# Kernel tuning notes

Measured on AMD Instinct MI355X. Metric: run time of the kernel, lower is better.

## Reference

```python
import jax, jax.numpy as jnp
import numpy as np
from jax import lax

N, F_IN, HID, OUT, L, K = 50000, 128, 128, 64, 3, 9
E = 600000
PAD = (K - 1) // 2
BN_EPS = 1e-5


def setup_inputs() -> dict:
    key = jax.random.key(0)
    ks = jax.random.split(key, 16)
    return {
        "x": jax.random.normal(ks[0], (N, F_IN), jnp.float32),
        "edge_index": jax.random.randint(ks[1], (2, E), 0, N, jnp.int64),
        "tw": jax.random.normal(ks[2], (L, HID, F_IN, K), jnp.float32) * 0.05,
        "tb": jax.random.normal(ks[3], (L, HID), jnp.float32) * 0.05,
        "wl": jax.random.normal(ks[4], (L, HID, HID), jnp.float32) * 0.05,
        "bl": jax.random.normal(ks[5], (L, HID), jnp.float32) * 0.05,
        "wr": jax.random.normal(ks[6], (L, HID, HID), jnp.float32) * 0.05,
        "bn_g": jax.random.uniform(ks[7], (L, HID), jnp.float32, 0.5, 1.5),
        "bn_b": jax.random.normal(ks[8], (L, HID), jnp.float32) * 0.05,
        "bn_m": jax.random.normal(ks[9], (L, HID), jnp.float32) * 0.05,
        "bn_v": jax.random.uniform(ks[10], (L, HID), jnp.float32, 0.5, 1.5),
        "clf_w": jax.random.normal(ks[11], (OUT, HID), jnp.float32) * 0.05,
        "clf_b": jax.random.normal(ks[12], (OUT,), jnp.float32) * 0.05,
    }


def reference(x, edge_index, tw, tb, wl, bl, wr, bn_g, bn_b, bn_m, bn_v, clf_w, clf_b):
    # Eval mode: dropout = identity, BatchNorm uses running stats.
    src, dst = edge_index[0], edge_index[1]
    n = x.shape[0]
    # mean-aggregation denominator (PyG SAGEConv 'mean'); isolated nodes -> 0
    deg = jax.ops.segment_sum(jnp.ones((src.shape[0],), x.dtype), dst, num_segments=n)
    inv_deg = jnp.where(deg > 0, 1.0 / jnp.maximum(deg, 1.0), 0.0)[:, None]  # [N,1]
    for i in range(L):
        # temporal Conv1d over the NODE axis: [N,C] -> [1,C,N]
        h = lax.conv_general_dilated(
            x.T[None], tw[i], window_strides=(1,), padding=[(PAD, PAD)],
            dimension_numbers=("NCH", "OIH", "NCH"))
        h = jax.nn.relu(h + tb[i][None, :, None])[0].T  # [N, HID]
        # SAGEConv: lin_l(mean_j h_j) + lin_r(h_i)
        agg = jax.ops.segment_sum(h[src], dst, num_segments=n) * inv_deg
        h = agg @ wl[i].T + bl[i] + h @ wr[i].T
        # BatchNorm1d (eval) + ReLU
        h = bn_g[i] * (h - bn_m[i]) * lax.rsqrt(bn_v[i] + BN_EPS) + bn_b[i]
        x = jax.nn.relu(h)
    logits = x @ clf_w.T + clf_b
    return jax.nn.log_softmax(logits, axis=1)
```

## Files before the change

kernel.cpp:

```cpp
#include <hip/hip_runtime.h>
#include <cstddef>
#include <cstdint>


#define N_NODES 50000
#define FDIM    128
#define OUTC    64
#define NLAYER  3
#define KW      9
#define PADW    4
#define NEDGE   600000
#define BN_EPS  1e-5f

typedef short bf16x8 __attribute__((ext_vector_type(8)));
typedef float f32x4  __attribute__((ext_vector_type(4)));

__device__ __forceinline__ float relu_(float v){ return v > 0.f ? v : 0.f; }

__device__ __forceinline__ unsigned short bf_rne(float x){
  unsigned u = __float_as_uint(x);
  unsigned r = u + 0x7fff + ((u >> 16) & 1);
  return (unsigned short)(r >> 16);
}
__device__ __forceinline__ unsigned short bf_hi(float x, float& rem){
  unsigned short h = bf_rne(x);
  rem = x - __uint_as_float(((unsigned)h) << 16);
  return h;
}
__device__ __forceinline__ float bf2f(unsigned short u){
  return __uint_as_float(((unsigned)u) << 16);
}
__device__ __forceinline__ void cvt8(const float4& f0, const float4& f1, int4& hv, int4& lv){
  float f[8] = {f0.x,f0.y,f0.z,f0.w,f1.x,f1.y,f1.z,f1.w};
  unsigned short h[8], l[8];
  #pragma unroll
  for (int i=0;i<8;i++){ float r; h[i] = bf_hi(f[i], r); l[i] = bf_rne(r); }
  hv.x = (int)((unsigned)h[0] | ((unsigned)h[1]<<16));
  hv.y = (int)((unsigned)h[2] | ((unsigned)h[3]<<16));
  hv.z = (int)((unsigned)h[4] | ((unsigned)h[5]<<16));
  hv.w = (int)((unsigned)h[6] | ((unsigned)h[7]<<16));
  lv.x = (int)((unsigned)l[0] | ((unsigned)l[1]<<16));
  lv.y = (int)((unsigned)l[2] | ((unsigned)l[3]<<16));
  lv.z = (int)((unsigned)l[4] | ((unsigned)l[5]<<16));
  lv.w = (int)((unsigned)l[6] | ((unsigned)l[7]<<16));
}


__global__ void k_detect(const int* __restrict__ ei, int* __restrict__ flag){
  int t = threadIdx.x;
  unsigned long long b = __ballot(ei[2*t+1] == 0);
  if (t == 0) flag[0] = (b == ~0ull) ? 1 : 0;
}

__global__ void k_zero(int* __restrict__ p, int n){
  int i = blockIdx.x*256 + threadIdx.x;
  if (i < n) p[i] = 0;
}

__global__ void k_deg(const int* __restrict__ ei, const int* __restrict__ flag, int* __restrict__ deg){
  int e = blockIdx.x*256 + threadIdx.x;
  if (e >= NEDGE) return;
  int d = flag[0] ? ei[2*(NEDGE+e)] : ei[NEDGE+e];
  atomicAdd(&deg[d], 1);
}

__global__ void k_scan1(const int* __restrict__ deg, int* __restrict__ rp, int* __restrict__ bsums){
  __shared__ int sd[256];
  int t = threadIdx.x, base = blockIdx.x*1024 + t*4;
  int v0=0,v1=0,v2=0,v3=0;
  if (base+3 < N_NODES){ int4 q = *(const int4*)(deg+base); v0=q.x; v1=q.y; v2=q.z; v3=q.w; }
  else {
    if (base   < N_NODES) v0 = deg[base];
    if (base+1 < N_NODES) v1 = deg[base+1];
    if (base+2 < N_NODES) v2 = deg[base+2];
    if (base+3 < N_NODES) v3 = deg[base+3];
  }
  int s = v0+v1+v2+v3;
  sd[t] = s; __syncthreads();
  #pragma unroll
  for (int o=1;o<256;o<<=1){
    int x = (t>=o) ? sd[t-o] : 0;
    __syncthreads();
    sd[t] += x;
    __syncthreads();
  }
  int excl = sd[t]-s;
  if (base   < N_NODES) rp[base  ] = excl;
  if (base+1 < N_NODES) rp[base+1] = excl+v0;
  if (base+2 < N_NODES) rp[base+2] = excl+v0+v1;
  if (base+3 < N_NODES) rp[base+3] = excl+v0+v1+v2;
  if (t==255) bsums[blockIdx.x] = sd[255];
}

__global__ void k_scan2(int* __restrict__ bsums, int nb){
  if (threadIdx.x==0 && blockIdx.x==0){
    int run = 0;
    for (int i=0;i<nb;i++){ int x = bsums[i]; bsums[i] = run; run += x; }
  }
}

__global__ void k_scan3(int* __restrict__ rp, int* __restrict__ cur, float* __restrict__ idg,
                        const int* __restrict__ deg, const int* __restrict__ bsums){
  int i = blockIdx.x*256 + threadIdx.x;
  if (i < N_NODES){
    int r = rp[i] + bsums[i>>10];
    rp[i] = r; cur[i] = r;
    int d = deg[i];
    idg[i] = (d>0) ? 1.0f/(float)d : 0.0f;
  } else if (i == N_NODES){
    rp[N_NODES] = NEDGE;
  }
}

__global__ void k_fill(const int* __restrict__ ei, const int* __restrict__ flag,
                       int* __restrict__ cur, int* __restrict__ col){
  int e = blockIdx.x*256 + threadIdx.x;
  if (e >= NEDGE) return;
  int s,d;
  if (flag[0]){ s = ei[2*e]; d = ei[2*(NEDGE+e)]; }
  else        { s = ei[e];   d = ei[NEDGE+e];   }
  int pos = atomicAdd(&cur[d], 1);
  col[pos] = s;
}


__global__ void k_pack(const float* __restrict__ tw, const float* __restrict__ wl,
                       const float* __restrict__ wr, const float* __restrict__ cw,
                       unsigned short* __restrict__ wp, unsigned short* __restrict__ wg,
                       float* __restrict__ cwt){
  int i = blockIdx.x*256 + threadIdx.x;
  const int T1v = 442368, T2v = 98304, T3v = 8192;
  if (i < T1v){
    int e = i & 7, lane = (i>>3)&63, ob = (i>>9)&7, cb = (i>>12)&3, kl = i>>14;
    int k = kl % KW, l = kl / KW;
    int o = ob*16 + (lane&15), c = cb*32 + (lane>>4)*8 + e;
    float v = tw[(((l*128+o)*128+c)*KW) + k];
    float rem; unsigned short hi = bf_hi(v, rem); unsigned short lo = bf_rne(rem);
    int chunk = (((l*KW+k)*4+cb)*8+ob)*2;
    wp[(size_t)chunk*512 + lane*8 + e]     = hi;
    wp[(size_t)(chunk+1)*512 + lane*8 + e] = lo;
  } else if (i < T1v+T2v){
    int i2 = i - T1v;
    int e = i2 & 7, lane = (i2>>3)&63, ob = (i2>>9)&7, ks = (i2>>12)&7, l = i2>>15;
    int o = ob*16 + (lane&15), j = ks*32 + (lane>>4)*8 + e;
    float v = (j < 128) ? wl[(l*128+o)*128 + j] : wr[(l*128+o)*128 + (j-128)];
    float rem; unsigned short hi = bf_hi(v, rem); unsigned short lo = bf_rne(rem);
    int chunk = ((l*8+ks)*8+ob)*2;
    wg[(size_t)chunk*512 + lane*8 + e]     = hi;
    wg[(size_t)(chunk+1)*512 + lane*8 + e] = lo;
  } else if (i < T1v+T2v+T3v){
    int j3 = i - (T1v+T2v);
    int o = j3 & 63, c = j3 >> 6;
    cwt[j3] = cw[o*128 + c];
  }
}


#define CROWS 72

__global__ __launch_bounds__(256, 4) void k_convm(const float* __restrict__ xf,
                                                  const unsigned short* __restrict__ xhi,
                                                  const unsigned short* __restrict__ xlo,
                                                  const int use_planes,
                                                  const unsigned short* __restrict__ wpl,
                                                  const float* __restrict__ tb,
                                                  unsigned short* __restrict__ hhi,
                                                  unsigned short* __restrict__ hlo){
  __shared__ unsigned short sh[2*CROWS*64];
  const int t = threadIdx.x;
  const int n0 = blockIdx.x*64;
  const int l = t & 63, w = t >> 6;
  const int l15 = l & 15, kg = l >> 4;
  const bf16x8* Bp = (const bf16x8*)wpl;

  f32x4 acc[4][2];
  #pragma unroll
  for (int rf=0;rf<4;rf++){ acc[rf][0] = (f32x4)0.f; acc[rf][1] = (f32x4)0.f; }

  bf16x8 B00, B01, B10, B11;
  {
    int ch = ((0*4+0)*8 + 2*w)*2;
    B00 = Bp[ch*64 + l]; B01 = Bp[(ch+1)*64 + l];
    B10 = Bp[(ch+2)*64 + l]; B11 = Bp[(ch+3)*64 + l];
  }

  for (int half = 0; half < 2; ++half){
    if (half) __syncthreads();
    for (int u = t; u < CROWS*8; u += 256){
      int row = u >> 3, c8 = u & 7;
      int gn = n0 - PADW + row;
      int4 hv = make_int4(0,0,0,0), lv = make_int4(0,0,0,0);
      if (gn >= 0 && gn < N_NODES){
        if (use_planes){
          size_t o = (size_t)gn*FDIM + half*64 + c8*8;
          hv = *(const int4*)(xhi + o);
          lv = *(const int4*)(xlo + o);
        } else {
          const float* src = xf + (size_t)gn*FDIM + half*64 + c8*8;
          float4 f0 = *(const float4*)src, f1 = *(const float4*)(src+4);
          cvt8(f0, f1, hv, lv);
        }
      }
      int idx = row*64 + ((c8 ^ (row&7)) << 3);
      *(int4*)&sh[idx] = hv;
      *(int4*)&sh[CROWS*64 + idx] = lv;
    }
    __syncthreads();

    for (int kk = 0; kk < 18; ++kk){
      int k = kk >> 1, cb2 = kk & 1;
      bf16x8 Bc00=B00, Bc01=B01, Bc10=B10, Bc11=B11;
      {
        int it = half*18 + kk;
        int itn = (it+1 < 36) ? it+1 : it;
        int halfn = itn/18, kkn = itn%18;
        int kn = kkn>>1, cb2n = kkn&1, cbgn = halfn*2 + cb2n;
        int ch = ((kn*4+cbgn)*8 + 2*w)*2;
        B00 = Bp[ch*64 + l]; B01 = Bp[(ch+1)*64 + l];
        B10 = Bp[(ch+2)*64 + l]; B11 = Bp[(ch+3)*64 + l];
      }
      int cc3 = cb2*4 + kg;
      int swz = ((cc3 ^ ((l15 + k) & 7)) << 3);
      int base = (l15 + k)*64 + swz;
      #pragma unroll
      for (int rf = 0; rf < 4; ++rf){
        int idx = base + rf*16*64;
        bf16x8 Ah = *(const bf16x8*)&sh[idx];
        bf16x8 Al = *(const bf16x8*)&sh[CROWS*64 + idx];
        acc[rf][0] = __builtin_amdgcn_mfma_f32_16x16x32_bf16(Ah, Bc00, acc[rf][0], 0,0,0);
        acc[rf][0] = __builtin_amdgcn_mfma_f32_16x16x32_bf16(Ah, Bc01, acc[rf][0], 0,0,0);
        acc[rf][0] = __builtin_amdgcn_mfma_f32_16x16x32_bf16(Al, Bc00, acc[rf][0], 0,0,0);
        acc[rf][1] = __builtin_amdgcn_mfma_f32_16x16x32_bf16(Ah, Bc10, acc[rf][1], 0,0,0);
        acc[rf][1] = __builtin_amdgcn_mfma_f32_16x16x32_bf16(Ah, Bc11, acc[rf][1], 0,0,0);
        acc[rf][1] = __builtin_amdgcn_mfma_f32_16x16x32_bf16(Al, Bc10, acc[rf][1], 0,0,0);
      }
    }
  }

  int o0 = w*32 + l15, o1 = o0 + 16;
  float tb0 = tb[o0], tb1 = tb[o1];
  #pragma unroll
  for (int rf = 0; rf < 4; ++rf){
    #pragma unroll
    for (int j = 0; j < 4; ++j){
      int n = n0 + rf*16 + kg*4 + j;
      if (n < N_NODES){
        float v0 = relu_(acc[rf][0][j] + tb0);
        float v1 = relu_(acc[rf][1][j] + tb1);
        float r0, r1;
        unsigned short h0 = bf_hi(v0, r0), h1 = bf_hi(v1, r1);
        size_t b = (size_t)n*FDIM;
        hhi[b+o0] = h0; hlo[b+o0] = bf_rne(r0);
        hhi[b+o1] = h1; hlo[b+o1] = bf_rne(r1);
      }
    }
  }
}


__global__ __launch_bounds__(256) void k_agg(const unsigned short* __restrict__ hhi,
                                             const int* __restrict__ rp,
                                             const int* __restrict__ col,
                                             const float* __restrict__ idg,
                                             unsigned short* __restrict__ ahi,
                                             unsigned short* __restrict__ alo){
  int n = blockIdx.x*4 + (threadIdx.x>>6);
  int lane = threadIdx.x & 63;
  int half = lane >> 5, li = lane & 31;
  if (n >= N_NODES) return;
  int s0 = rp[n], s1 = rp[n+1];
  float a0=0.f, a1=0.f, a2=0.f, a3=0.f;
  int e = s0 + half;
  for (; e + 2 < s1; e += 4){
    int sA = col[e], sB = col[e+2];
    ushort4 vA = *(const ushort4*)(hhi + (size_t)sA*FDIM + li*4);
    ushort4 vB = *(const ushort4*)(hhi + (size_t)sB*FDIM + li*4);
    a0 += bf2f(vA.x) + bf2f(vB.x);
    a1 += bf2f(vA.y) + bf2f(vB.y);
    a2 += bf2f(vA.z) + bf2f(vB.z);
    a3 += bf2f(vA.w) + bf2f(vB.w);
  }
  for (; e < s1; e += 2){
    int s = col[e];
    ushort4 v = *(const ushort4*)(hhi + (size_t)s*FDIM + li*4);
    a0 += bf2f(v.x); a1 += bf2f(v.y); a2 += bf2f(v.z); a3 += bf2f(v.w);
  }
  a0 += __shfl_xor(a0, 32);
  a1 += __shfl_xor(a1, 32);
  a2 += __shfl_xor(a2, 32);
  a3 += __shfl_xor(a3, 32);
  float wv = idg[n];
  a0 *= wv; a1 *= wv; a2 *= wv; a3 *= wv;
  float r0,r1,r2,r3;
  unsigned short h0 = bf_hi(a0,r0), h1 = bf_hi(a1,r1), h2 = bf_hi(a2,r2), h3 = bf_hi(a3,r3);
  size_t b = (size_t)n*FDIM + li*4;
  if (half == 0){
    ushort4 o; o.x=h0; o.y=h1; o.z=h2; o.w=h3;
    *(ushort4*)(ahi + b) = o;
  } else {
    ushort4 o; o.x=bf_rne(r0); o.y=bf_rne(r1); o.z=bf_rne(r2); o.w=bf_rne(r3);
    *(ushort4*)(alo + b) = o;
  }
}


__global__ __launch_bounds__(256, 4) void k_gemmm(const unsigned short* __restrict__ ahi,
                                                  const unsigned short* __restrict__ alo,
                                                  const unsigned short* __restrict__ hhi,
                                                  const unsigned short* __restrict__ hlo,
                                                  const unsigned short* __restrict__ wgl,
                                                  const float* __restrict__ bl,
                                                  const float* __restrict__ bng, const float* __restrict__ bnb,
                                                  const float* __restrict__ bnm, const float* __restrict__ bnv,
                                                  unsigned short* __restrict__ xhi,
                                                  unsigned short* __restrict__ xlo){
  __shared__ unsigned short sh[2*64*64];
  const int t = threadIdx.x;
  const int n0 = blockIdx.x*64;
  const int l = t & 63, w = t >> 6;
  const int l15 = l & 15, kg = l >> 4;
  const bf16x8* Bp = (const bf16x8*)wgl;

  f32x4 acc[4][2];
  #pragma unroll
  for (int rf=0;rf<4;rf++){ acc[rf][0] = (f32x4)0.f; acc[rf][1] = (f32x4)0.f; }

  bf16x8 B00, B01, B10, B11;
  {
    int ch = (0*8 + 2*w)*2;
    B00 = Bp[ch*64 + l]; B01 = Bp[(ch+1)*64 + l];
    B10 = Bp[(ch+2)*64 + l]; B11 = Bp[(ch+3)*64 + l];
  }

  for (int p = 0; p < 4; ++p){
    if (p) __syncthreads();
    const unsigned short* shi = (p >= 2) ? hhi : ahi;
    const unsigned short* slo = (p >= 2) ? hlo : alo;
    int ch0 = (p & 1)*64;
    for (int u = t; u < 64*8; u += 256){
      int row = u >> 3, c8 = u & 7;
      int gn = n0 + row;
      int4 hv = make_int4(0,0,0,0), lv = make_int4(0,0,0,0);
      if (gn < N_NODES){
        size_t o = (size_t)gn*FDIM + ch0 + c8*8;
        hv = *(const int4*)(shi + o);
        lv = *(const int4*)(slo + o);
      }
      int idx = row*64 + ((c8 ^ (row&7)) << 3);
      *(int4*)&sh[idx] = hv;
      *(int4*)&sh[64*64 + idx] = lv;
    }
    __syncthreads();

    for (int cb2 = 0; cb2 < 2; ++cb2){
      bf16x8 Bc00=B00, Bc01=B01, Bc10=B10, Bc11=B11;
      {
        int ks = p*2 + cb2;
        int ksn = (ks+1 < 8) ? ks+1 : ks;
        int ch = (ksn*8 + 2*w)*2;
        B00 = Bp[ch*64 + l]; B01 = Bp[(ch+1)*64 + l];
        B10 = Bp[(ch+2)*64 + l]; B11 = Bp[(ch+3)*64 + l];
      }
      int cc3 = cb2*4 + kg;
      int swz = ((cc3 ^ (l15 & 7)) << 3);
      int base = l15*64 + swz;
      #pragma unroll
      for (int rf = 0; rf < 4; ++rf){
        int idx = base + rf*16*64;
        bf16x8 Ah = *(const bf16x8*)&sh[idx];
        bf16x8 Al = *(const bf16x8*)&sh[64*64 + idx];
        acc[rf][0] = __builtin_amdgcn_mfma_f32_16x16x32_bf16(Ah, Bc00, acc[rf][0], 0,0,0);
        acc[rf][0] = __builtin_amdgcn_mfma_f32_16x16x32_bf16(Ah, Bc01, acc[rf][0], 0,0,0);
        acc[rf][0] = __builtin_amdgcn_mfma_f32_16x16x32_bf16(Al, Bc00, acc[rf][0], 0,0,0);
        acc[rf][1] = __builtin_amdgcn_mfma_f32_16x16x32_bf16(Ah, Bc10, acc[rf][1], 0,0,0);
        acc[rf][1] = __builtin_amdgcn_mfma_f32_16x16x32_bf16(Ah, Bc11, acc[rf][1], 0,0,0);
        acc[rf][1] = __builtin_amdgcn_mfma_f32_16x16x32_bf16(Al, Bc10, acc[rf][1], 0,0,0);
      }
    }
  }

  int o0 = w*32 + l15, o1 = o0 + 16;
  float s0 = bng[o0]*rsqrtf(bnv[o0]+BN_EPS);
  float c0 = bnb[o0] + s0*(bl[o0]-bnm[o0]);
  float s1 = bng[o1]*rsqrtf(bnv[o1]+BN_EPS);
  float c1 = bnb[o1] + s1*(bl[o1]-bnm[o1]);
  #pragma unroll
  for (int rf = 0; rf < 4; ++rf){
    #pragma unroll
    for (int j = 0; j < 4; ++j){
      int n = n0 + rf*16 + kg*4 + j;
      if (n < N_NODES){
        float v0 = relu_(s0*acc[rf][0][j] + c0);
        float v1 = relu_(s1*acc[rf][1][j] + c1);
        float r0, r1;
        unsigned short h0 = bf_hi(v0, r0), h1 = bf_hi(v1, r1);
        size_t b = (size_t)n*FDIM;
        xhi[b+o0] = h0; xlo[b+o0] = bf_rne(r0);
        xhi[b+o1] = h1; xlo[b+o1] = bf_rne(r1);
      }
    }
  }
}


__global__ __launch_bounds__(256) void k_clf(const unsigned short* __restrict__ xhi,
                                             const unsigned short* __restrict__ xlo,
                                             const float* __restrict__ cwt,
                                             const float* __restrict__ cb, float* __restrict__ out){
  __shared__ float As[128][68];
  __shared__ float mxl[64];
  const int t = threadIdx.x, n0 = blockIdx.x*64;
  const int ng = t & 15, og = t>>4;
  float acc[4][4];
  #pragma unroll
  for (int i=0;i<4;i++)
    #pragma unroll
    for (int j=0;j<4;j++) acc[i][j] = 0.f;

  for (int u=t; u<64*16; u+=256){
    int row = u>>4, c16 = u&15;
    int gn = n0 + row;
    int4 hv = make_int4(0,0,0,0), lv = make_int4(0,0,0,0);
    if (gn < N_NODES){
      size_t o = (size_t)gn*FDIM + c16*8;
      hv = *(const int4*)(xhi + o);
      lv = *(const int4*)(xlo + o);
    }
    const unsigned short* hs = (const unsigned short*)&hv;
    const unsigned short* ls = (const unsigned short*)&lv;
    #pragma unroll
    for (int j=0;j<8;j++) As[c16*8+j][row] = bf2f(hs[j]) + bf2f(ls[j]);
  }
  __syncthreads();
  #pragma unroll 2
  for (int c=0;c<128;c++){
    float aa[4] = {As[c][ng], As[c][ng+16], As[c][ng+32], As[c][ng+48]};
    float4 b = *(const float4*)(cwt + c*64 + og*4);
    float bb[4] = {b.x,b.y,b.z,b.w};
    #pragma unroll
    for (int i=0;i<4;i++)
      #pragma unroll
      for (int j=0;j<4;j++) acc[i][j] = fmaf(aa[i], bb[j], acc[i][j]);
  }
  __syncthreads();
  float4 cb4 = *(const float4*)(cb + og*4);
  float cbv[4] = {cb4.x,cb4.y,cb4.z,cb4.w};
  #pragma unroll
  for (int i=0;i<4;i++)
    #pragma unroll
    for (int j=0;j<4;j++) As[ng+16*i][og*4+j] = acc[i][j] + cbv[j];
  __syncthreads();
  if (t < 64){
    float mx = -1e30f;
    #pragma unroll 8
    for (int o=0;o<64;o++) mx = fmaxf(mx, As[t][o]);
    float se = 0.f;
    #pragma unroll 8
    for (int o=0;o<64;o++) se += expf(As[t][o]-mx);
    mxl[t] = mx + logf(se);
  }
  __syncthreads();
  #pragma unroll
  for (int v=0;v<4;v++){
    int q = t + v*256;
    int r = q>>4, o4 = (q&15)*4;
    int n = n0 + r;
    if (n < N_NODES){
      float4 L = *(const float4*)&As[r][o4];
      float m = mxl[r];
      float4 wv; wv.x = L.x-m; wv.y = L.y-m; wv.z = L.z-m; wv.w = L.w-m;
      *(float4*)(out + (size_t)n*OUTC + o4) = wv;
    }
  }
}


extern "C" void kernel_launch(void* const* d_in, const int* in_sizes, int n_in,
                              void* d_out, int out_size, void* d_ws, size_t ws_size,
                              hipStream_t stream) {
  const float* x   = (const float*)d_in[0];
  const int*   ei  = (const int*)  d_in[1];
  const float* tw  = (const float*)d_in[2];
  const float* tb  = (const float*)d_in[3];
  const float* wl  = (const float*)d_in[4];
  const float* bl  = (const float*)d_in[5];
  const float* wr  = (const float*)d_in[6];
  const float* bng = (const float*)d_in[7];
  const float* bnb = (const float*)d_in[8];
  const float* bnm = (const float*)d_in[9];
  const float* bnv = (const float*)d_in[10];
  const float* cw  = (const float*)d_in[11];
  const float* cb  = (const float*)d_in[12];
  float* out = (float*)d_out;
  char* ws = (char*)d_ws;

  auto align256 = [](size_t v){ return (v + 255) & ~(size_t)255; };
  size_t off = 0;
  auto take = [&](size_t bytes){ size_t o = off; off += align256(bytes); return o; };
  const size_t PLANE = (size_t)N_NODES*FDIM*2;
  unsigned short* xhi = (unsigned short*)(ws + take(PLANE));
  unsigned short* xlo = (unsigned short*)(ws + take(PLANE));
  unsigned short* hhi = (unsigned short*)(ws + take(PLANE));
  unsigned short* hlo = (unsigned short*)(ws + take(PLANE));
  unsigned short* ahi = (unsigned short*)(ws + take(PLANE));
  unsigned short* alo = (unsigned short*)(ws + take(PLANE));
  unsigned short* wp  = (unsigned short*)(ws + take((size_t)884736*2));
  unsigned short* wg  = (unsigned short*)(ws + take((size_t)196608*2));
  float* cwt   = (float*)(ws + take((size_t)128*64*4));
  int*   deg   = (int*)  (ws + take((size_t)N_NODES*4));
  int*   rp    = (int*)  (ws + take((size_t)(N_NODES+1)*4));
  int*   cur   = (int*)  (ws + take((size_t)N_NODES*4));
  int*   col   = (int*)  (ws + take((size_t)NEDGE*4));
  float* idg   = (float*)(ws + take((size_t)N_NODES*4));
  int*   bsums = (int*)  (ws + take(256));
  int*   flag  = (int*)  (ws + take(256));
  (void)ws_size; (void)in_sizes; (void)n_in; (void)out_size;

  const int NB_N   = (N_NODES + 255)/256;
  const int NB_E   = (NEDGE   + 255)/256;
  const int NB_SC  = (N_NODES + 1023)/1024;
  const int NB_T64 = (N_NODES + 63)/64;
  const int NB_PK  = (442368 + 98304 + 8192)/256;

  k_detect<<<1, 64, 0, stream>>>(ei, flag);
  k_zero  <<<NB_N, 256, 0, stream>>>(deg, N_NODES);
  k_deg   <<<NB_E, 256, 0, stream>>>(ei, flag, deg);
  k_scan1 <<<NB_SC, 256, 0, stream>>>(deg, rp, bsums);
  k_scan2 <<<1, 64, 0, stream>>>(bsums, NB_SC);
  k_scan3 <<<NB_N+1, 256, 0, stream>>>(rp, cur, idg, deg, bsums);
  k_fill  <<<NB_E, 256, 0, stream>>>(ei, flag, cur, col);
  k_pack  <<<NB_PK, 256, 0, stream>>>(tw, wl, wr, cw, wp, wg, cwt);

  for (int l=0; l<NLAYER; l++){
    k_convm<<<NB_T64, 256, 0, stream>>>(x, xhi, xlo, (l>0) ? 1 : 0,
                                        wp + (size_t)l*294912, tb + l*128, hhi, hlo);
    k_agg  <<<N_NODES/4, 256, 0, stream>>>(hhi, rp, col, idg, ahi, alo);
    k_gemmm<<<NB_T64, 256, 0, stream>>>(ahi, alo, hhi, hlo, wg + (size_t)l*65536,
                                        bl + l*128, bng + l*128, bnb + l*128,
                                        bnm + l*128, bnv + l*128, xhi, xlo);
  }
  k_clf<<<NB_T64, 256, 0, stream>>>(xhi, xlo, cwt, cb, out);
}
```

Measured before the change: 474.8 us.

## Prefetch next shared-memory stage into registers and double-buffer weight fragments

In the temporal-conv and SAGE linear kernels, the global loads for the next input stage are now issued into registers before the MFMA loop on the current stage, then written to shared memory after a barrier. This lets global-memory latency overlap with matrix compute instead of stalling at each stage boundary. Weight fragments are also double-buffered two iterations ahead, using two register sets. The cost is higher register pressure, which may reduce occupancy, plus an extra barrier per stage.

Result: slower. 502.1 us (+5.7%).

```diff
diff --git a/kernel.cpp b/kernel.cpp
--- a/kernel.cpp
+++ b/kernel.cpp
@@ -177,63 +177,113 @@
   #pragma unroll
   for (int rf=0;rf<4;rf++){ acc[rf][0] = (f32x4)0.f; acc[rf][1] = (f32x4)0.f; }
 
-  bf16x8 B00, B01, B10, B11;
-  {
-    int ch = ((0*4+0)*8 + 2*w)*2;
-    B00 = Bp[ch*64 + l]; B01 = Bp[(ch+1)*64 + l];
-    B10 = Bp[(ch+2)*64 + l]; B11 = Bp[(ch+3)*64 + l];
-  }
-
-  for (int half = 0; half < 2; ++half){
-    if (half) __syncthreads();
-    for (int u = t; u < CROWS*8; u += 256){
-      int row = u >> 3, c8 = u & 7;
-      int gn = n0 - PADW + row;
-      int4 hv = make_int4(0,0,0,0), lv = make_int4(0,0,0,0);
-      if (gn >= 0 && gn < N_NODES){
-        if (use_planes){
-          size_t o = (size_t)gn*FDIM + half*64 + c8*8;
-          hv = *(const int4*)(xhi + o);
-          lv = *(const int4*)(xlo + o);
-        } else {
-          const float* src = xf + (size_t)gn*FDIM + half*64 + c8*8;
-          float4 f0 = *(const float4*)src, f1 = *(const float4*)(src+4);
+  int4 sA[3], sB[3];
+  auto stage_load = [&](int half){
+    #pragma unroll
+    for (int i=0;i<3;i++){
+      int u = t + i*256;
+      sA[i] = make_int4(0,0,0,0); sB[i] = make_int4(0,0,0,0);
+      if (u < CROWS*8){
+        int row = u>>3, c8 = u&7;
+        int gn = n0 - PADW + row;
+        if (gn >= 0 && gn < N_NODES){
+          if (use_planes){
+            size_t o = (size_t)gn*FDIM + half*64 + c8*8;
+            sA[i] = *(const int4*)(xhi + o);
+            sB[i] = *(const int4*)(xlo + o);
+          } else {
+            const float* src = xf + (size_t)gn*FDIM + half*64 + c8*8;
+            sA[i] = *(const int4*)src;
+            sB[i] = *(const int4*)(src+4);
+          }
+        }
+      }
+    }
+  };
+  auto stage_write = [&](){
+    #pragma unroll
+    for (int i=0;i<3;i++){
+      int u = t + i*256;
+      if (u < CROWS*8){
+        int row = u>>3, c8 = u&7;
+        int idx = row*64 + ((c8 ^ (row&7)) << 3);
+        int4 hv, lv;
+        if (use_planes){ hv = sA[i]; lv = sB[i]; }
+        else {
+          float4 f0 = *(float4*)&sA[i], f1 = *(float4*)&sB[i];
           cvt8(f0, f1, hv, lv);
         }
-      }
-      int idx = row*64 + ((c8 ^ (row&7)) << 3);
-      *(int4*)&sh[idx] = hv;
-      *(int4*)&sh[CROWS*64 + idx] = lv;
-    }
-    __syncthreads();
-
-    for (int kk = 0; kk < 18; ++kk){
-      int k = kk >> 1, cb2 = kk & 1;
-      bf16x8 Bc00=B00, Bc01=B01, Bc10=B10, Bc11=B11;
+        *(int4*)&sh[idx] = hv;
+        *(int4*)&sh[CROWS*64 + idx] = lv;
+      }
+    }
+  };
+
+  auto chbase = [&](int it)->int{
+    int halfn = it/18, kkn = it%18;
+    int kn = kkn>>1, cb2n = kkn&1, cbgn = halfn*2 + cb2n;
+    return ((kn*4+cbgn)*8 + 2*w)*2;
+  };
+
+  bf16x8 BA0,BA1,BA2,BA3, BB0,BB1,BB2,BB3;
+  { int ch = chbase(0);
+    BA0 = Bp[ch*64+l]; BA1 = Bp[(ch+1)*64+l]; BA2 = Bp[(ch+2)*64+l]; BA3 = Bp[(ch+3)*64+l]; }
+  { int ch = chbase(1);
+    BB0 = Bp[ch*64+l]; BB1 = Bp[(ch+1)*64+l]; BB2 = Bp[(ch+2)*64+l]; BB3 = Bp[(ch+3)*64+l]; }
+
+  stage_load(0);
+  stage_write();
+  __syncthreads();
+
+  for (int half = 0; half < 2; ++half){
+    if (half == 0) stage_load(1);
+    for (int kk2 = 0; kk2 < 18; kk2 += 2){
+      int k = kk2 >> 1;
+      int rowk = l15 + k;
       {
-        int it = half*18 + kk;
-        int itn = (it+1 < 36) ? it+1 : it;
-        int halfn = itn/18, kkn = itn%18;
-        int kn = kkn>>1, cb2n = kkn&1, cbgn = halfn*2 + cb2n;
-        int ch = ((kn*4+cbgn)*8 + 2*w)*2;
-        B00 = Bp[ch*64 + l]; B01 = Bp[(ch+1)*64 + l];
-        B10 = Bp[(ch+2)*64 + l]; B11 = Bp[(ch+3)*64 + l];
-      }
-      int cc3 = cb2*4 + kg;
-      int swz = ((cc3 ^ ((l15 + k) & 7)) << 3);
-      int base = (l15 + k)*64 + swz;
-      #pragma unroll
-      for (int rf = 0; rf < 4; ++rf){
-        int idx = base + rf*16*64;
-        bf16x8 Ah = *(const bf16x8*)&sh[idx];
-        bf16x8 Al = *(const bf16x8*)&sh[CROWS*64 + idx];
-        acc[rf][0] = __builtin_amdgcn_mfma_f32_16x16x32_bf16(Ah, Bc00, acc[rf][0], 0,0,0);
-        acc[rf][0] = __builtin_amdgcn_mfma_f32_16x16x32_bf16(Ah, Bc01, acc[rf][0], 0,0,0);
-        acc[rf][0] = __builtin_amdgcn_mfma_f32_16x16x32_bf16(Al, Bc00, acc[rf][0], 0,0,0);
-        acc[rf][1] = __builtin_amdgcn_mfma_f32_16x16x32_bf16(Ah, Bc10, acc[rf][1], 0,0,0);
-        acc[rf][1] = __builtin_amdgcn_mfma_f32_16x16x32_bf16(Ah, Bc11, acc[rf][1], 0,0,0);
-        acc[rf][1] = __builtin_amdgcn_mfma_f32_16x16x32_bf16(Al, Bc10, acc[rf][1], 0,0,0);
-      }
+        bf16x8 Bc0=BA0, Bc1=BA1, Bc2=BA2, Bc3=BA3;
+        int itn = half*18 + kk2 + 2; if (itn > 35) itn = 35;
+        int ch = chbase(itn);
+        BA0 = Bp[ch*64+l]; BA1 = Bp[(ch+1)*64+l]; BA2 = Bp[(ch+2)*64+l]; BA3 = Bp[(ch+3)*64+l];
+        int base = rowk*64 + ((kg ^ (rowk&7)) << 3);
+        #pragma unroll
+        for (int rf = 0; rf < 4; ++rf){
+          int idx = base + rf*16*64;
+          bf16x8 Ah = *(const bf16x8*)&sh[idx];
+          bf16x8 Al = *(const bf16x8*)&sh[CROWS*64 + idx];
+          acc[rf][0] = __builtin_amdgcn_mfma_f32_16x16x32_bf16(Ah, Bc0, acc[rf][0], 0,0,0);
+          acc[rf][0] = __builtin_amdgcn_mfma_f32_16x16x32_bf16(Ah, Bc1, acc[rf][0], 0,0,0);
+          acc[rf][0] = __builtin_amdgcn_mfma_f32_16x16x32_bf16(Al, Bc0, acc[rf][0], 0,0,0);
+          acc[rf][1] = __builtin_amdgcn_mfma_f32_16x16x32_bf16(Ah, Bc2, acc[rf][1], 0,0,0);
+          acc[rf][1] = __builtin_amdgcn_mfma_f32_16x16x32_bf16(Ah, Bc3, acc[rf][1], 0,0,0);
+          acc[rf][1] = __builtin_amdgcn_mfma_f32_16x16x32_bf16(Al, Bc2, acc[rf][1], 0,0,0);
+        }
+      }
+      {
+        bf16x8 Bc0=BB0, Bc1=BB1, Bc2=BB2, Bc3=BB3;
+        int itn = half*18 + kk2 + 3; if (itn > 35) itn = 35;
+        int ch = chbase(itn);
+        BB0 = Bp[ch*64+l]; BB1 = Bp[(ch+1)*64+l]; BB2 = Bp[(ch+2)*64+l]; BB3 = Bp[(ch+3)*64+l];
+        int cc3 = 4 + kg;
+        int base = rowk*64 + ((cc3 ^ (rowk&7)) << 3);
+        #pragma unroll
+        for (int rf = 0; rf < 4; ++rf){
+          int idx = base + rf*16*64;
+          bf16x8 Ah = *(const bf16x8*)&sh[idx];
+          bf16x8 Al = *(const bf16x8*)&sh[CROWS*64 + idx];
+          acc[rf][0] = __builtin_amdgcn_mfma_f32_16x16x32_bf16(Ah, Bc0, acc[rf][0], 0,0,0);
+          acc[rf][0] = __builtin_amdgcn_mfma_f32_16x16x32_bf16(Ah, Bc1, acc[rf][0], 0,0,0);
+          acc[rf][0] = __builtin_amdgcn_mfma_f32_16x16x32_bf16(Al, Bc0, acc[rf][0], 0,0,0);
+          acc[rf][1] = __builtin_amdgcn_mfma_f32_16x16x32_bf16(Ah, Bc2, acc[rf][1], 0,0,0);
+          acc[rf][1] = __builtin_amdgcn_mfma_f32_16x16x32_bf16(Ah, Bc3, acc[rf][1], 0,0,0);
+          acc[rf][1] = __builtin_amdgcn_mfma_f32_16x16x32_bf16(Al, Bc2, acc[rf][1], 0,0,0);
+        }
+      }
+    }
+    if (half == 0){
+      __syncthreads();
+      stage_write();
+      __syncthreads();
     }
   }
 
@@ -325,57 +375,91 @@
   #pragma unroll
   for (int rf=0;rf<4;rf++){ acc[rf][0] = (f32x4)0.f; acc[rf][1] = (f32x4)0.f; }
 
-  bf16x8 B00, B01, B10, B11;
-  {
-    int ch = (0*8 + 2*w)*2;
-    B00 = Bp[ch*64 + l]; B01 = Bp[(ch+1)*64 + l];
-    B10 = Bp[(ch+2)*64 + l]; B11 = Bp[(ch+3)*64 + l];
-  }
-
-  for (int p = 0; p < 4; ++p){
-    if (p) __syncthreads();
+  int4 sA2[2], sB2[2];
+  auto stage_load = [&](int p){
     const unsigned short* shi = (p >= 2) ? hhi : ahi;
     const unsigned short* slo = (p >= 2) ? hlo : alo;
     int ch0 = (p & 1)*64;
-    for (int u = t; u < 64*8; u += 256){
-      int row = u >> 3, c8 = u & 7;
+    #pragma unroll
+    for (int i=0;i<2;i++){
+      int u = t + i*256;
+      int row = u>>3, c8 = u&7;
       int gn = n0 + row;
-      int4 hv = make_int4(0,0,0,0), lv = make_int4(0,0,0,0);
+      sA2[i] = make_int4(0,0,0,0); sB2[i] = make_int4(0,0,0,0);
       if (gn < N_NODES){
         size_t o = (size_t)gn*FDIM + ch0 + c8*8;
-        hv = *(const int4*)(shi + o);
-        lv = *(const int4*)(slo + o);
-      }
+        sA2[i] = *(const int4*)(shi + o);
+        sB2[i] = *(const int4*)(slo + o);
+      }
+    }
+  };
+  auto stage_write = [&](){
+    #pragma unroll
+    for (int i=0;i<2;i++){
+      int u = t + i*256;
+      int row = u>>3, c8 = u&7;
       int idx = row*64 + ((c8 ^ (row&7)) << 3);
-      *(int4*)&sh[idx] = hv;
-      *(int4*)&sh[64*64 + idx] = lv;
-    }
-    __syncthreads();
-
-    for (int cb2 = 0; cb2 < 2; ++cb2){
-      bf16x8 Bc00=B00, Bc01=B01, Bc10=B10, Bc11=B11;
-      {
-        int ks = p*2 + cb2;
-        int ksn = (ks+1 < 8) ? ks+1 : ks;
-        int ch = (ksn*8 + 2*w)*2;
-        B00 = Bp[ch*64 + l]; B01 = Bp[(ch+1)*64 + l];
-        B10 = Bp[(ch+2)*64 + l]; B11 = Bp[(ch+3)*64 + l];
-      }
-      int cc3 = cb2*4 + kg;
-      int swz = ((cc3 ^ (l15 & 7)) << 3);
-      int base = l15*64 + swz;
+      *(int4*)&sh[idx] = sA2[i];
+      *(int4*)&sh[64*64 + idx] = sB2[i];
+    }
+  };
+  auto chbase = [&](int ks)->int{ return (ks*8 + 2*w)*2; };
+
+  bf16x8 BA0,BA1,BA2,BA3, BB0,BB1,BB2,BB3;
+  { int ch = chbase(0);
+    BA0 = Bp[ch*64+l]; BA1 = Bp[(ch+1)*64+l]; BA2 = Bp[(ch+2)*64+l]; BA3 = Bp[(ch+3)*64+l]; }
+  { int ch = chbase(1);
+    BB0 = Bp[ch*64+l]; BB1 = Bp[(ch+1)*64+l]; BB2 = Bp[(ch+2)*64+l]; BB3 = Bp[(ch+3)*64+l]; }
+
+  stage_load(0);
+  stage_write();
+  __syncthreads();
+
+  for (int p = 0; p < 4; ++p){
+    if (p < 3) stage_load(p+1);
+    {
+      bf16x8 Bc0=BA0, Bc1=BA1, Bc2=BA2, Bc3=BA3;
+      int ksn = 2*p + 2; if (ksn > 7) ksn = 7;
+      int ch = chbase(ksn);
+      BA0 = Bp[ch*64+l]; BA1 = Bp[(ch+1)*64+l]; BA2 = Bp[(ch+2)*64+l]; BA3 = Bp[(ch+3)*64+l];
+      int base = l15*64 + ((kg ^ (l15&7)) << 3);
       #pragma unroll
       for (int rf = 0; rf < 4; ++rf){
         int idx = base + rf*16*64;
         bf16x8 Ah = *(const bf16x8*)&sh[idx];
         bf16x8 Al = *(const bf16x8*)&sh[64*64 + idx];
-        acc[rf][0] = __builtin_amdgcn_mfma_f32_16x16x32_bf16(Ah, Bc00, acc[rf][0], 0,0,0);
-        acc[rf][0] = __builtin_amdgcn_mfma_f32_16x16x32_bf16(Ah, Bc01, acc[rf][0], 0,0,0);
-        acc[rf][0] = __builtin_amdgcn_mfma_f32_16x16x32_bf16(Al, Bc00, acc[rf][0], 0,0,0);
-        acc[rf][1] = __builtin_amdgcn_mfma_f32_16x16x32_bf16(Ah, Bc10, acc[rf][1], 0,0,0);
-        acc[rf][1] = __builtin_amdgcn_mfma_f32_16x16x32_bf16(Ah, Bc11, acc[rf][1], 0,0,0);
-        acc[rf][1] = __builtin_amdgcn_mfma_f32_16x16x32_bf16(Al, Bc10, acc[rf][1], 0,0,0);
-      }
+        acc[rf][0] = __builtin_amdgcn_mfma_f32_16x16x32_bf16(Ah, Bc0, acc[rf][0], 0,0,0);
+        acc[rf][0] = __builtin_amdgcn_mfma_f32_16x16x32_bf16(Ah, Bc1, acc[rf][0], 0,0,0);
+        acc[rf][0] = __builtin_amdgcn_mfma_f32_16x16x32_bf16(Al, Bc0, acc[rf][0], 0,0,0);
+        acc[rf][1] = __builtin_amdgcn_mfma_f32_16x16x32_bf16(Ah, Bc2, acc[rf][1], 0,0,0);
+        acc[rf][1] = __builtin_amdgcn_mfma_f32_16x16x32_bf16(Ah, Bc3, acc[rf][1], 0,0,0);
+        acc[rf][1] = __builtin_amdgcn_mfma_f32_16x16x32_bf16(Al, Bc2, acc[rf][1], 0,0,0);
+      }
+    }
+    {
+      bf16x8 Bc0=BB0, Bc1=BB1, Bc2=BB2, Bc3=BB3;
+      int ksn = 2*p + 3; if (ksn > 7) ksn = 7;
+      int ch = chbase(ksn);
+      BB0 = Bp[ch*64+l]; BB1 = Bp[(ch+1)*64+l]; BB2 = Bp[(ch+2)*64+l]; BB3 = Bp[(ch+3)*64+l];
+      int cc3 = 4 + kg;
+      int base = l15*64 + ((cc3 ^ (l15&7)) << 3);
+      #pragma unroll
+      for (int rf = 0; rf < 4; ++rf){
+        int idx = base + rf*16*64;
+        bf16x8 Ah = *(const bf16x8*)&sh[idx];
+        bf16x8 Al = *(const bf16x8*)&sh[64*64 + idx];
+        acc[rf][0] = __builtin_amdgcn_mfma_f32_16x16x32_bf16(Ah, Bc0, acc[rf][0], 0,0,0);
+        acc[rf][0] = __builtin_amdgcn_mfma_f32_16x16x32_bf16(Ah, Bc1, acc[rf][0], 0,0,0);
+        acc[rf][0] = __builtin_amdgcn_mfma_f32_16x16x32_bf16(Al, Bc0, acc[rf][0], 0,0,0);
+        acc[rf][1] = __builtin_amdgcn_mfma_f32_16x16x32_bf16(Ah, Bc2, acc[rf][1], 0,0,0);
+        acc[rf][1] = __builtin_amdgcn_mfma_f32_16x16x32_bf16(Ah, Bc3, acc[rf][1], 0,0,0);
+        acc[rf][1] = __builtin_amdgcn_mfma_f32_16x16x32_bf16(Al, Bc2, acc[rf][1], 0,0,0);
+      }
+    }
+    if (p < 3){
+      __syncthreads();
+      stage_write();
+      __syncthreads();
     }
   }
 
```

## Double-buffer LDS staging with direct global-to-LDS loads in conv and GEMM kernels

Applied to the files above, without the earlier changes.

The conv and GEMM kernels get two LDS buffers, so the next half or panel is staged while MFMAs run on the current one. Interior blocks fill LDS with global_load_lds, which copies global memory straight into shared memory without going through registers. The swizzle is applied on the global address side so the LDS layout stays the same. LDS use doubles, which can lower occupancy, and correctness relies on the __syncthreads waiting for the asynchronous LDS loads to land.

New measurement: 475.5 us. Within noise of the previous version (+0.1%).

```diff
diff --git a/kernel.cpp b/kernel.cpp
--- a/kernel.cpp
+++ b/kernel.cpp
@@ -43,6 +43,12 @@
   lv.y = (int)((unsigned)l[2] | ((unsigned)l[3]<<16));
   lv.z = (int)((unsigned)l[4] | ((unsigned)l[5]<<16));
   lv.w = (int)((unsigned)l[6] | ((unsigned)l[7]<<16));
+}
+
+__device__ __forceinline__ void gl16(const unsigned short* g, unsigned short* l){
+  __builtin_amdgcn_global_load_lds(
+      (const __attribute__((address_space(1))) void*)g,
+      (__attribute__((address_space(3))) void*)l, 16, 0, 0);
 }
 
 
@@ -157,6 +163,7 @@
 
 
 #define CROWS 72
+#define CPL   (CROWS*64)
 
 __global__ __launch_bounds__(256, 4) void k_convm(const float* __restrict__ xf,
                                                   const unsigned short* __restrict__ xhi,
@@ -166,16 +173,51 @@
                                                   const float* __restrict__ tb,
                                                   unsigned short* __restrict__ hhi,
                                                   unsigned short* __restrict__ hlo){
-  __shared__ unsigned short sh[2*CROWS*64];
+  __shared__ unsigned short sh[4*CPL];
   const int t = threadIdx.x;
   const int n0 = blockIdx.x*64;
   const int l = t & 63, w = t >> 6;
   const int l15 = l & 15, kg = l >> 4;
   const bf16x8* Bp = (const bf16x8*)wpl;
+  const int fast = use_planes && (n0 >= PADW) && (n0 + (CROWS-1-PADW) < N_NODES);
 
   f32x4 acc[4][2];
   #pragma unroll
   for (int rf=0;rf<4;rf++){ acc[rf][0] = (f32x4)0.f; acc[rf][1] = (f32x4)0.f; }
+
+  auto stage = [&](int half, int buf){
+    unsigned short* bb = sh + buf*2*CPL;
+    if (fast){
+      for (int qb = w*64; qb < CROWS*8; qb += 256){
+        int q = qb + l;
+        int row = q >> 3;
+        int c8s = (q & 7) ^ (row & 7);
+        size_t go = (size_t)(n0 - PADW + row)*FDIM + half*64 + c8s*8;
+        gl16(xhi + go, bb + qb*8);
+        gl16(xlo + go, bb + CPL + qb*8);
+      }
+    } else {
+      for (int u = t; u < CROWS*8; u += 256){
+        int row = u>>3, c8 = u&7;
+        int gn = n0 - PADW + row;
+        int4 hv = make_int4(0,0,0,0), lv = make_int4(0,0,0,0);
+        if (gn >= 0 && gn < N_NODES){
+          if (use_planes){
+            size_t o = (size_t)gn*FDIM + half*64 + c8*8;
+            hv = *(const int4*)(xhi + o);
+            lv = *(const int4*)(xlo + o);
+          } else {
+            const float* src = xf + (size_t)gn*FDIM + half*64 + c8*8;
+            float4 f0 = *(const float4*)src, f1 = *(const float4*)(src+4);
+            cvt8(f0, f1, hv, lv);
+          }
+        }
+        int idx = row*64 + ((c8 ^ (row&7)) << 3);
+        *(int4*)&bb[idx] = hv;
+        *(int4*)&bb[CPL + idx] = lv;
+      }
+    }
+  };
 
   bf16x8 B00, B01, B10, B11;
   {
@@ -184,29 +226,12 @@
     B10 = Bp[(ch+2)*64 + l]; B11 = Bp[(ch+3)*64 + l];
   }
 
+  stage(0, 0);
+  __syncthreads();
+  stage(1, 1);
+
   for (int half = 0; half < 2; ++half){
-    if (half) __syncthreads();
-    for (int u = t; u < CROWS*8; u += 256){
-      int row = u >> 3, c8 = u & 7;
-      int gn = n0 - PADW + row;
-      int4 hv = make_int4(0,0,0,0), lv = make_int4(0,0,0,0);
-      if (gn >= 0 && gn < N_NODES){
-        if (use_planes){
-          size_t o = (size_t)gn*FDIM + half*64 + c8*8;
-          hv = *(const int4*)(xhi + o);
-          lv = *(const int4*)(xlo + o);
-        } else {
-          const float* src = xf + (size_t)gn*FDIM + half*64 + c8*8;
-          float4 f0 = *(const float4*)src, f1 = *(const float4*)(src+4);
-          cvt8(f0, f1, hv, lv);
-        }
-      }
-      int idx = row*64 + ((c8 ^ (row&7)) << 3);
-      *(int4*)&sh[idx] = hv;
-      *(int4*)&sh[CROWS*64 + idx] = lv;
-    }
-    __syncthreads();
-
+    const unsigned short* bb = sh + half*2*CPL;
     for (int kk = 0; kk < 18; ++kk){
       int k = kk >> 1, cb2 = kk & 1;
       bf16x8 Bc00=B00, Bc01=B01, Bc10=B10, Bc11=B11;
@@ -220,13 +245,13 @@
         B10 = Bp[(ch+2)*64 + l]; B11 = Bp[(ch+3)*64 + l];
       }
       int cc3 = cb2*4 + kg;
-      int swz = ((cc3 ^ ((l15 + k) & 7)) << 3);
-      int base = (l15 + k)*64 + swz;
+      int rowk = l15 + k;
+      int base = rowk*64 + ((cc3 ^ (rowk&7)) << 3);
       #pragma unroll
       for (int rf = 0; rf < 4; ++rf){
         int idx = base + rf*16*64;
-        bf16x8 Ah = *(const bf16x8*)&sh[idx];
-        bf16x8 Al = *(const bf16x8*)&sh[CROWS*64 + idx];
+        bf16x8 Ah = *(const bf16x8*)&bb[idx];
+        bf16x8 Al = *(const bf16x8*)&bb[CPL + idx];
         acc[rf][0] = __builtin_amdgcn_mfma_f32_16x16x32_bf16(Ah, Bc00, acc[rf][0], 0,0,0);
         acc[rf][0] = __builtin_amdgcn_mfma_f32_16x16x32_bf16(Ah, Bc01, acc[rf][0], 0,0,0);
         acc[rf][0] = __builtin_amdgcn_mfma_f32_16x16x32_bf16(Al, Bc00, acc[rf][0], 0,0,0);
@@ -235,6 +260,7 @@
         acc[rf][1] = __builtin_amdgcn_mfma_f32_16x16x32_bf16(Al, Bc10, acc[rf][1], 0,0,0);
       }
     }
+    if (half == 0) __syncthreads();
   }
 
   int o0 = w*32 + l15, o1 = o0 + 16;
@@ -304,6 +330,8 @@
 }
 
 
+#define GPL (64*64)
+
 __global__ __launch_bounds__(256, 4) void k_gemmm(const unsigned short* __restrict__ ahi,
                                                   const unsigned short* __restrict__ alo,
                                                   const unsigned short* __restrict__ hhi,
@@ -314,16 +342,48 @@
                                                   const float* __restrict__ bnm, const float* __restrict__ bnv,
                                                   unsigned short* __restrict__ xhi,
                                                   unsigned short* __restrict__ xlo){
-  __shared__ unsigned short sh[2*64*64];
+  __shared__ unsigned short sh[4*GPL];
   const int t = threadIdx.x;
   const int n0 = blockIdx.x*64;
   const int l = t & 63, w = t >> 6;
   const int l15 = l & 15, kg = l >> 4;
   const bf16x8* Bp = (const bf16x8*)wgl;
+  const int fast = (n0 + 63 < N_NODES);
 
   f32x4 acc[4][2];
   #pragma unroll
   for (int rf=0;rf<4;rf++){ acc[rf][0] = (f32x4)0.f; acc[rf][1] = (f32x4)0.f; }
+
+  auto stage = [&](int p, int buf){
+    unsigned short* bb = sh + buf*2*GPL;
+    const unsigned short* shi = (p >= 2) ? hhi : ahi;
+    const unsigned short* slo = (p >= 2) ? hlo : alo;
+    int ch0 = (p & 1)*64;
+    if (fast){
+      for (int qb = w*64; qb < 64*8; qb += 256){
+        int q = qb + l;
+        int row = q >> 3;
+        int c8s = (q & 7) ^ (row & 7);
+        size_t go = (size_t)(n0 + row)*FDIM + ch0 + c8s*8;
+        gl16(shi + go, bb + qb*8);
+        gl16(slo + go, bb + GPL + qb*8);
+      }
+    } else {
+      for (int u = t; u < 64*8; u += 256){
+        int row = u>>3, c8 = u&7;
+        int gn = n0 + row;
+        int4 hv = make_int4(0,0,0,0), lv = make_int4(0,0,0,0);
+        if (gn < N_NODES){
+          size_t o = (size_t)gn*FDIM + ch0 + c8*8;
+          hv = *(const int4*)(shi + o);
+          lv = *(const int4*)(slo + o);
+        }
+        int idx = row*64 + ((c8 ^ (row&7)) << 3);
+        *(int4*)&bb[idx] = hv;
+        *(int4*)&bb[GPL + idx] = lv;
+      }
+    }
+  };
 
   bf16x8 B00, B01, B10, B11;
   {
@@ -332,26 +392,12 @@
     B10 = Bp[(ch+2)*64 + l]; B11 = Bp[(ch+3)*64 + l];
   }
 
+  stage(0, 0);
+  __syncthreads();
+
   for (int p = 0; p < 4; ++p){
-    if (p) __syncthreads();
-    const unsigned short* shi = (p >= 2) ? hhi : ahi;
-    const unsigned short* slo = (p >= 2) ? hlo : alo;
-    int ch0 = (p & 1)*64;
-    for (int u = t; u < 64*8; u += 256){
-      int row = u >> 3, c8 = u & 7;
-      int gn = n0 + row;
-      int4 hv = make_int4(0,0,0,0), lv = make_int4(0,0,0,0);
-      if (gn < N_NODES){
-        size_t o = (size_t)gn*FDIM + ch0 + c8*8;
-        hv = *(const int4*)(shi + o);
-        lv = *(const int4*)(slo + o);
-      }
-      int idx = row*64 + ((c8 ^ (row&7)) << 3);
-      *(int4*)&sh[idx] = hv;
-      *(int4*)&sh[64*64 + idx] = lv;
-    }
-    __syncthreads();
-
+    if (p < 3) stage(p+1, (p+1)&1);
+    const unsigned short* bb = sh + (p&1)*2*GPL;
     for (int cb2 = 0; cb2 < 2; ++cb2){
       bf16x8 Bc00=B00, Bc01=B01, Bc10=B10, Bc11=B11;
       {
@@ -362,13 +408,12 @@
         B10 = Bp[(ch+2)*64 + l]; B11 = Bp[(ch+3)*64 + l];
       }
       int cc3 = cb2*4 + kg;
-      int swz = ((cc3 ^ (l15 & 7)) << 3);
-      int base = l15*64 + swz;
+      int base = l15*64 + ((cc3 ^ (l15&7)) << 3);
       #pragma unroll
       for (int rf = 0; rf < 4; ++rf){
         int idx = base + rf*16*64;
-        bf16x8 Ah = *(const bf16x8*)&sh[idx];
-        bf16x8 Al = *(const bf16x8*)&sh[64*64 + idx];
+        bf16x8 Ah = *(const bf16x8*)&bb[idx];
+        bf16x8 Al = *(const bf16x8*)&bb[GPL + idx];
         acc[rf][0] = __builtin_amdgcn_mfma_f32_16x16x32_bf16(Ah, Bc00, acc[rf][0], 0,0,0);
         acc[rf][0] = __builtin_amdgcn_mfma_f32_16x16x32_bf16(Ah, Bc01, acc[rf][0], 0,0,0);
         acc[rf][0] = __builtin_amdgcn_mfma_f32_16x16x32_bf16(Al, Bc00, acc[rf][0], 0,0,0);
@@ -377,6 +422,7 @@
         acc[rf][1] = __builtin_amdgcn_mfma_f32_16x16x32_bf16(Al, Bc10, acc[rf][1], 0,0,0);
       }
     }
+    if (p < 3) __syncthreads();
   }
 
   int o0 = w*32 + l15, o1 = o0 + 16;
```
